# Performance work log

Measured on AMD Instinct MI355X. Metric: run time of the kernel, lower is better.

## Reference

```python
import jax, jax.numpy as jnp
import numpy as np

# Static architecture constants (from init_kwargs)
NUM_AREAS = 4
E_PER = 512          # excitatory units per area
I_PER = 128          # inhibitory units per area
H = NUM_AREAS * (E_PER + I_PER)   # 2560 hidden units
E_SIZE = NUM_AREAS * E_PER        # 2048 = int(0.8 * H)
NUM_OBJS = 2
IN_UNITS = 64
IN_SIZE = NUM_OBJS * IN_UNITS     # 128
ALPHA = 0.02 / 0.1                # dt_x / tau_x


def _build_masks():
    # Recurrent block-connectivity: tridiagonal area graph (adjacent areas connected)
    rec = np.eye(NUM_AREAS) + np.eye(NUM_AREAS, k=1) + np.eye(NUM_AREAS, k=-1)
    ee = np.kron(rec, np.ones((E_PER, E_PER)))
    ie = np.kron(rec, np.ones((I_PER, E_PER)))
    ei = np.kron(np.eye(NUM_AREAS), np.ones((E_PER, I_PER)))
    ii = np.kron(np.eye(NUM_AREAS), np.ones((I_PER, I_PER)))
    conn_rec = np.block([[ee, ei], [ie, ii]])  # rows/cols ordered [all-E | all-I]
    # Dale sign mask: first E_SIZE columns excitatory (+1), rest inhibitory (-1)
    sign = np.concatenate([np.ones(E_SIZE), -np.ones(H - E_SIZE)])[None, :]
    mask_rec = conn_rec * sign
    np.fill_diagonal(mask_rec, 0.0)  # remove_diag=True in h2h EILinear
    # Input connectivity: only area 0 receives external input (e_prop=1 -> all +1)
    in_mask = np.zeros((NUM_AREAS, NUM_OBJS)); in_mask[0, :] = 1.0
    in_e = np.kron(in_mask, np.ones((E_PER, IN_UNITS)))
    in_i = np.kron(in_mask, np.ones((I_PER, IN_UNITS)))
    mask_in = np.vstack([in_e, in_i])
    return jnp.asarray(mask_rec, jnp.float32), jnp.asarray(mask_in, jnp.float32)

MASK_REC, MASK_IN = _build_masks()


def retanh(x):
    return jnp.tanh(jax.nn.relu(x))


def setup_inputs() -> dict:
    key = jax.random.key(0)
    k1, k2, k3 = jax.random.split(key, 3)
    T, B = 32, 64
    x = jax.random.normal(k1, (T, B, IN_SIZE), dtype=jnp.float32)
    # positive-ish inits (original uses gamma; scale ~ 1/sqrt(fan-in))
    W_in = jax.random.uniform(k2, (H, IN_SIZE), dtype=jnp.float32) * 0.02
    W_rec = jax.random.uniform(k3, (H, H), dtype=jnp.float32) * (1.0 / np.sqrt(H))
    b_rec = jnp.zeros((H,), jnp.float32)
    state0 = jnp.zeros((B, H), jnp.float32)
    return {"x": x, "W_in": W_in, "W_rec": W_rec, "b_rec": b_rec, "state0": state0}


def reference(x, W_in, W_rec, b_rec, state0):
    # Effective weights: pos_function='abs' applied to raw weights, then sign/conn mask
    Wr = jnp.abs(W_rec) * MASK_REC          # [H, H]
    Wi = jnp.abs(W_in) * MASK_IN            # [H, IN_SIZE]

    def step(state, xt):
        out = retanh(state)                                # activation of old state
        total = out @ Wr.T + jax.nn.relu(xt) @ Wi.T + b_rec  # h2h(output) + x2h(relu(x)) + bias
        new_state = state * (1.0 - ALPHA) + ALPHA * total    # leaky integration (sigma=0)
        return new_state, retanh(new_state)

    _, outputs = jax.lax.scan(step, state0, x)  # outputs: [T, B, H]
    return outputs
```

## Files before the change

### kernel.cpp

```cpp
#include <hip/hip_runtime.h>
#include <math.h>

#define HH   2560
#define ESZ  2048
#define BB   64
#define TT   32
#define INSZ 128
constexpr float ALPHA_C = 0.2f;

typedef unsigned short ushort_t;
typedef __attribute__((ext_vector_type(8))) unsigned short u16x8;
typedef __attribute__((ext_vector_type(4))) float f32x4;

__device__ __forceinline__ float retanh_f(float v) { return tanhf(fmaxf(v, 0.f)); }
__device__ __forceinline__ ushort_t f2bf(float f) {
    unsigned u = __float_as_uint(f);
    return (ushort_t)((u + 0x7fffu + ((u >> 16) & 1u)) >> 16);
}

__device__ __forceinline__ int area_ne(int a)  { return (a == 1 || a == 2) ? 1536 : 1024; }
__device__ __forceinline__ int area_elo(int a) { return (a > 0 ? a - 1 : 0) << 9; }

__global__ __launch_bounds__(256) void wf_pack8(const float* __restrict__ Wrec,
                                                const float* __restrict__ Win,
                                                ushort_t* __restrict__ WF) {
    int idx = blockIdx.x * 256 + threadIdx.x;
    int l = idx & 63;
    int t = idx >> 6;
    int kc = t % 52, mt = t / 52;
    int area = mt / 40, local = mt - area * 40;
    int ridx = local * 16 + (l & 15);
    int h = (ridx < 512) ? ((area << 9) + ridx) : (ESZ + (area << 7) + (ridx - 512));
    int p0 = kc * 32 + ((l >> 4) << 3);
    int ne = area_ne(area), elo = area_elo(area);
    int nrec = ne + 128;
    int ntot = nrec + (area == 0 ? 128 : 0);
    u16x8 o;
#pragma unroll
    for (int j = 0; j < 8; j++) {
        int p = p0 + j;
        float w = 0.f;
        if (p < ne)        { int c = elo + p;                      w = (c == h) ? 0.f :  fabsf(Wrec[(size_t)h * HH + c]); }
        else if (p < nrec) { int c = ESZ + (area << 7) + (p - ne); w = (c == h) ? 0.f : -fabsf(Wrec[(size_t)h * HH + c]); }
        else if (p < ntot) { w = fabsf(Win[(size_t)h * INSZ + (p - nrec)]); }
        o[j] = f2bf(w);
    }
    *(u16x8*)(WF + ((size_t)t * 512 + l * 8)) = o;
}

__global__ __launch_bounds__(256) void xf_pack(const float* __restrict__ x,
                                               ushort_t* __restrict__ xF) {
    int idx = blockIdx.x * 256 + threadIdx.x;
    int j = idx & 7, l = (idx >> 3) & 63;
    int nt = (idx >> 9) & 3, kc = (idx >> 11) & 3, t = idx >> 13;
    int b = nt * 16 + (l & 15);
    int k = kc * 32 + ((l >> 4) << 3) + j;
    xF[idx] = f2bf(fmaxf(x[((size_t)t * BB + b) * INSZ + k], 0.f));
}

__device__ __forceinline__ void act_store(ushort_t* actF, int a, int p, int b, ushort_t v) {
    int kc = p >> 5, kk = p & 31;
    int lane = ((kk >> 3) << 4) + (b & 15);
    actF[(((a * 52 + kc) << 2) + (b >> 4)) * 512 + lane * 8 + (kk & 7)] = v;
}
__device__ __forceinline__ void scatter_act(ushort_t* actF, int h, int b, ushort_t v) {
    if (h < ESZ) {
        int ae = h >> 9;
        int alo = ae > 0 ? ae - 1 : 0, ahi = ae < 3 ? ae + 1 : 3;
        for (int a = alo; a <= ahi; a++) act_store(actF, a, h - area_elo(a), b, v);
    } else {
        int ai = (h - ESZ) >> 7;
        act_store(actF, ai, area_ne(ai) + (h - (ESZ + (ai << 7))), b, v);
    }
}

__global__ __launch_bounds__(256) void init3(const float* __restrict__ state0,
                                             float* __restrict__ stateT,
                                             ushort_t* __restrict__ actF) {
    int idx = blockIdx.x * 256 + threadIdx.x;
    int b = idx / HH, h = idx - b * HH;
    float s = state0[idx];
    int r = (h < ESZ) ? ((h >> 9) * 640 + (h & 511))
                      : (((h - ESZ) >> 7) * 640 + 512 + ((h - ESZ) & 127));
    stateT[r * BB + b] = s;
    scatter_act(actF, h, b, f2bf(retanh_f(s)));
}

__global__ __launch_bounds__(256) void step9(
    const ushort_t* __restrict__ WF,
    const ushort_t* __restrict__ actF_in,
    ushort_t* __restrict__ actF_out,
    const ushort_t* __restrict__ xFt,
    const float* __restrict__ brec,
    float* __restrict__ stateT,
    float* __restrict__ out_t)
{
    __shared__ float part[4 * 256];
    const int tid = threadIdx.x, lane = tid & 63, wv = tid >> 6;
    const int bid = blockIdx.x;
    const int area = (bid >> 1) & 3;
    const int nt   = ((bid >> 2) & 2) | (bid & 1);
    const int ml   = bid >> 4;
    const int mt   = area * 40 + ml;
    const int r0   = area * 640 + ml * 16;

    f32x4 acc = {0.f, 0.f, 0.f, 0.f};
    const ushort_t* aptr = WF + ((size_t)mt * 52 + wv) * 512 + lane * 8;
    const ushort_t* bptr = actF_in + (((size_t)area * 52 + wv) * 4 + nt) * 512 + lane * 8;
    const ushort_t* xptr = xFt + ((wv * 4) + nt) * 512 + lane * 8;

#define KLOOP(NIT, HASX)                                                     \
    {                                                                        \
        u16x8 af[NIT], bf[NIT];                                              \
        _Pragma("unroll")                                                    \
        for (int i = 0; i < (NIT); i++) {                                    \
            af[i] = *(const u16x8*)(aptr + (size_t)i * 2048);                \
            bf[i] = ((HASX) && i == (NIT) - 1)                               \
                        ? *(const u16x8*)xptr                                \
                        : *(const u16x8*)(bptr + (size_t)i * 8192);          \
        }                                                                    \
        _Pragma("unroll")                                                    \
        for (int i = 0; i < (NIT); i++)                                      \
            asm volatile("v_mfma_f32_16x16x32_bf16 %0, %1, %2, %0"           \
                         : "+v"(acc) : "v"(af[i]), "v"(bf[i]));              \
    }

    if (area == 0)      KLOOP(10, true)
    else if (area == 3) KLOOP(9,  false)
    else                KLOOP(13, false)
#undef KLOOP

    asm volatile("s_nop 7\n\ts_nop 7" : "+v"(acc));

#pragma unroll
    for (int i = 0; i < 4; i++)
        part[wv * 256 + (lane & 15) * 16 + ((lane >> 4) << 2) + i] = acc[i];
    __syncthreads();

    {
        const int mm = tid & 15, nn = tid >> 4;
        float s = part[nn * 16 + mm] + part[256 + nn * 16 + mm]
                + part[512 + nn * 16 + mm] + part[768 + nn * 16 + mm];
        const int b = nt * 16 + nn;
        const int ridx = ml * 16 + mm;
        const int h = (ridx < 512) ? ((area << 9) + ridx)
                                   : (ESZ + (area << 7) + (ridx - 512));
        const int r = r0 + mm;
        float st = stateT[r * BB + b];
        float ns = st * (1.f - ALPHA_C) + ALPHA_C * (s + brec[h]);
        stateT[r * BB + b] = ns;
        float o = retanh_f(ns);
        out_t[(size_t)b * HH + h] = o;
        scatter_act(actF_out, h, b, f2bf(o));
    }
}

__device__ __forceinline__ void area_params(int area, int& e_lo, int& n_e,
                                            int& i_lo, int& n_rec, int& n_tot) {
    e_lo = (area > 0 ? area - 1 : 0) << 9;
    int e_hi = ((area < 3 ? area + 1 : 3) + 1) << 9;
    n_e = e_hi - e_lo;
    i_lo = ESZ + (area << 7);
    n_rec = n_e + 128;
    n_tot = n_rec + (area == 0 ? INSZ : 0);
}
__device__ __forceinline__ int row_h(int area, int idx) {
    return (idx < 512) ? ((area << 9) + idx) : (ESZ + (area << 7) + (idx - 512));
}
__global__ __launch_bounds__(256) void init_state2(const float* __restrict__ state0,
                                                   float* __restrict__ stateT,
                                                   float* __restrict__ act0) {
    int idx = blockIdx.x * 256 + threadIdx.x;
    int b = idx / HH, h = idx - b * HH;
    float s = state0[idx];
    int r = (h < ESZ) ? ((h >> 9) * 640 + (h & 511))
                      : (((h - ESZ) >> 7) * 640 + 512 + ((h - ESZ) & 127));
    stateT[r * BB + b] = s;
    act0[((h >> 1) << 7) + b * 2 + (h & 1)] = retanh_f(s);
}
__global__ __launch_bounds__(1024, 4) void step_raw(
    const float* __restrict__ W, const float* __restrict__ Win,
    const float* __restrict__ brec, const float* __restrict__ x_t,
    const float* __restrict__ actIn, float* __restrict__ actOut,
    float* __restrict__ stateT, float* __restrict__ out_t)
{
    __shared__ float part[16 * 680];
    const int tid = threadIdx.x, lane = tid & 63, wv = tid >> 6;
    const int area = blockIdx.x >> 6;
    const int rb = (blockIdx.x & 63) * 10;
    int e_lo, n_e, i_lo, n_rec, n_tot;
    area_params(area, e_lo, n_e, i_lo, n_rec, n_tot);
    const int r0 = area * 640 + rb;
    const int C = n_tot >> 4;
    float2 acc[10];
#pragma unroll
    for (int j = 0; j < 10; j++) acc[j] = make_float2(0.f, 0.f);
    for (int c = wv; c < C; c += 16) {
        const int p0 = c << 4;
        float2 av[8];
        int cbase;
        if (p0 < n_rec) {
            cbase = (p0 < n_e) ? (e_lo + p0) : (i_lo + (p0 - n_e));
            const float* ap = actIn + ((cbase >> 1) << 7) + lane * 2;
#pragma unroll
            for (int i = 0; i < 8; i++) av[i] = *(const float2*)(ap + (i << 7));
        } else {
            cbase = -1;
            const int k0 = p0 - n_rec;
            const float4* xp = (const float4*)(x_t + lane * INSZ + k0);
#pragma unroll
            for (int q = 0; q < 4; q++) {
                float4 v = xp[q];
                av[2 * q]     = make_float2(fmaxf(v.x, 0.f), fmaxf(v.y, 0.f));
                av[2 * q + 1] = make_float2(fmaxf(v.z, 0.f), fmaxf(v.w, 0.f));
            }
        }
#pragma unroll
        for (int j = 0; j < 10; j++) {
            const int h = row_h(area, rb + j);
            const float sgn = (cbase >= 0 && p0 >= n_e) ? -1.f : 1.f;
            const float* wr = (cbase >= 0) ? (W + (size_t)h * HH + cbase)
                                           : (Win + (size_t)h * INSZ + (p0 - n_rec));
#pragma unroll
            for (int i = 0; i < 8; i++) {
                acc[j].x = fmaf(sgn * fabsf(wr[2 * i]),     av[i].x, acc[j].x);
                acc[j].y = fmaf(sgn * fabsf(wr[2 * i + 1]), av[i].y, acc[j].y);
            }
        }
    }
#pragma unroll
    for (int j = 0; j < 10; j++)
        part[wv * 680 + j * 68 + lane] = acc[j].x + acc[j].y;
    __syncthreads();
    int j = -1, b = 0;
    if (tid < 512)      { b = tid >> 3;      j = tid & 7; }
    else if (tid < 640) { int u = tid - 512; b = u >> 1;  j = 8 + (u & 1); }
    if (j >= 0) {
        const int h = row_h(area, rb + j);
        float s = 0.f;
#pragma unroll
        for (int w16 = 0; w16 < 16; w16++) s += part[w16 * 680 + j * 68 + b];
        float sgn = (h < ESZ) ? 1.f : -1.f;
        s -= sgn * fabsf(W[(size_t)h * HH + h]) * actIn[((h >> 1) << 7) + b * 2 + (h & 1)];
        const int r = r0 + j;
        float st = stateT[r * BB + b];
        float ns = st * (1.f - ALPHA_C) + ALPHA_C * (s + brec[h]);
        stateT[r * BB + b] = ns;
        float o = retanh_f(ns);
        out_t[(size_t)b * HH + h] = o;
        actOut[((h >> 1) << 7) + b * 2 + (h & 1)] = o;
    }
}

extern "C" void kernel_launch(void* const* d_in, const int* in_sizes, int n_in,
                              void* d_out, int out_size, void* d_ws, size_t ws_size,
                              hipStream_t stream) {
    const float* x      = (const float*)d_in[0];
    const float* W_in   = (const float*)d_in[1];
    const float* W_rec  = (const float*)d_in[2];
    const float* b_rec  = (const float*)d_in[3];
    const float* state0 = (const float*)d_in[4];
    float* out = (float*)d_out;

    const size_t WFn = (size_t)160 * 52 * 512;
    const size_t xFn = (size_t)TT * 8192;
    const size_t aFn = (size_t)4 * 52 * 4 * 512;
    const size_t need = (WFn + xFn + 2 * aFn) * 2 + (size_t)HH * BB * 4;

    if (ws_size >= need) {
        ushort_t* WF   = (ushort_t*)d_ws;
        ushort_t* xF   = WF + WFn;
        ushort_t* actA = xF + xFn;
        ushort_t* actB = actA + aFn;
        float* stateT  = (float*)(actB + aFn);

        wf_pack8<<<2080, 256, 0, stream>>>(W_rec, W_in, WF);
        xf_pack<<<1024, 256, 0, stream>>>(x, xF);
        init3<<<640, 256, 0, stream>>>(state0, stateT, actA);
        for (int t = 0; t < TT; t++) {
            ushort_t* ai = (t & 1) ? actB : actA;
            ushort_t* ao = (t & 1) ? actA : actB;
            step9<<<640, 256, 0, stream>>>(WF, ai, ao, xF + (size_t)t * 8192,
                                           b_rec, stateT, out + (size_t)t * BB * HH);
        }
    } else {
        float* ws = (float*)d_ws;
        const size_t bufElems = (size_t)HH * BB;
        float* stateT = ws;
        float* actA   = stateT + bufElems;
        float* actB   = actA + bufElems;
        init_state2<<<(BB * HH) / 256, 256, 0, stream>>>(state0, stateT, actA);
        for (int t = 0; t < TT; t++) {
            const float* ai = (t & 1) ? actB : actA;
            float* ao       = (t & 1) ? actA : actB;
            step_raw<<<256, 1024, 0, stream>>>(W_rec, W_in, b_rec,
                                               x + (size_t)t * BB * INSZ,
                                               ai, ao, stateT, out + (size_t)t * BB * HH);
        }
    }
}
```

Measured before the change: 286.9 us.

## Fuse all timesteps into one persistent kernel with flag-based grid barrier

Replaces the 32 per-timestep launches with a single persistent kernel of 160 blocks, one per 16-row M tile. Each block covers all four batch tiles and keeps its weight fragments and state in registers across steps. Steps are synchronised through per-block release flags polled with agent-scope atomics. This removes launch overhead and repeated weight and state loads, at the cost of fewer blocks (less parallelism), a spin-wait barrier with a guard limit, and reliance on all 160 blocks being co-resident.

```diff
diff --git a/kernel.cpp b/kernel.cpp
--- a/kernel.cpp
+++ b/kernel.cpp
@@ -76,7 +76,10 @@
 
 __global__ __launch_bounds__(256) void init3(const float* __restrict__ state0,
                                              float* __restrict__ stateT,
-                                             ushort_t* __restrict__ actF) {
+                                             ushort_t* __restrict__ actF,
+                                             unsigned* __restrict__ flags) {
+    if (blockIdx.x == 0 && threadIdx.x < 192)
+        flags[threadIdx.x] = (threadIdx.x < 160) ? 0u : 0xFFFFFFFFu;
     int idx = blockIdx.x * 256 + threadIdx.x;
     int b = idx / HH, h = idx - b * HH;
     float s = state0[idx];
@@ -86,73 +89,127 @@
     scatter_act(actF, h, b, f2bf(retanh_f(s)));
 }
 
-__global__ __launch_bounds__(256) void step9(
+template<int NIT, bool HASX>
+__device__ __forceinline__ void run_steps(
     const ushort_t* __restrict__ WF,
-    const ushort_t* __restrict__ actF_in,
-    ushort_t* __restrict__ actF_out,
-    const ushort_t* __restrict__ xFt,
-    const float* __restrict__ brec,
-    float* __restrict__ stateT,
-    float* __restrict__ out_t)
+    ushort_t* __restrict__ actA, ushort_t* __restrict__ actB,
+    const ushort_t* __restrict__ xF, const float* __restrict__ brec,
+    const float* __restrict__ stateT, float* __restrict__ out,
+    unsigned* __restrict__ flags, float* part, int mt, int area)
 {
-    __shared__ float part[4 * 256];
     const int tid = threadIdx.x, lane = tid & 63, wv = tid >> 6;
-    const int bid = blockIdx.x;
-    const int area = (bid >> 1) & 3;
-    const int nt   = ((bid >> 2) & 2) | (bid & 1);
-    const int ml   = bid >> 4;
-    const int mt   = area * 40 + ml;
-    const int r0   = area * 640 + ml * 16;
-
-    f32x4 acc = {0.f, 0.f, 0.f, 0.f};
-    const ushort_t* aptr = WF + ((size_t)mt * 52 + wv) * 512 + lane * 8;
-    const ushort_t* bptr = actF_in + (((size_t)area * 52 + wv) * 4 + nt) * 512 + lane * 8;
-    const ushort_t* xptr = xFt + ((wv * 4) + nt) * 512 + lane * 8;
-
-#define KLOOP(NIT, HASX)                                                     \
-    {                                                                        \
-        u16x8 af[NIT], bf[NIT];                                              \
-        _Pragma("unroll")                                                    \
-        for (int i = 0; i < (NIT); i++) {                                    \
-            af[i] = *(const u16x8*)(aptr + (size_t)i * 2048);                \
-            bf[i] = ((HASX) && i == (NIT) - 1)                               \
-                        ? *(const u16x8*)xptr                                \
-                        : *(const u16x8*)(bptr + (size_t)i * 8192);          \
-        }                                                                    \
-        _Pragma("unroll")                                                    \
-        for (int i = 0; i < (NIT); i++)                                      \
-            asm volatile("v_mfma_f32_16x16x32_bf16 %0, %1, %2, %0"           \
-                         : "+v"(acc) : "v"(af[i]), "v"(bf[i]));              \
-    }
-
-    if (area == 0)      KLOOP(10, true)
-    else if (area == 3) KLOOP(9,  false)
-    else                KLOOP(13, false)
-#undef KLOOP
-
-    asm volatile("s_nop 7\n\ts_nop 7" : "+v"(acc));
-
-#pragma unroll
-    for (int i = 0; i < 4; i++)
-        part[wv * 256 + (lane & 15) * 16 + ((lane >> 4) << 2) + i] = acc[i];
-    __syncthreads();
-
+    const int ml = mt - area * 40;
+
+    u16x8 af[NIT];
     {
-        const int mm = tid & 15, nn = tid >> 4;
-        float s = part[nn * 16 + mm] + part[256 + nn * 16 + mm]
-                + part[512 + nn * 16 + mm] + part[768 + nn * 16 + mm];
-        const int b = nt * 16 + nn;
-        const int ridx = ml * 16 + mm;
-        const int h = (ridx < 512) ? ((area << 9) + ridx)
-                                   : (ESZ + (area << 7) + (ridx - 512));
-        const int r = r0 + mm;
-        float st = stateT[r * BB + b];
-        float ns = st * (1.f - ALPHA_C) + ALPHA_C * (s + brec[h]);
-        stateT[r * BB + b] = ns;
-        float o = retanh_f(ns);
-        out_t[(size_t)b * HH + h] = o;
-        scatter_act(actF_out, h, b, f2bf(o));
-    }
+        const ushort_t* aptr = WF + ((size_t)mt * 52 + wv) * 512 + lane * 8;
+#pragma unroll
+        for (int i = 0; i < NIT; i++) af[i] = *(const u16x8*)(aptr + (size_t)i * 2048);
+    }
+
+    const int mm = tid & 15, nn = tid >> 4;
+    const int ridx = ml * 16 + mm;
+    const int h = (ridx < 512) ? ((area << 9) + ridx) : (ESZ + (area << 7) + (ridx - 512));
+    const int r = area * 640 + ml * 16 + mm;
+    const float bh = brec[h];
+    float st[4];
+#pragma unroll
+    for (int nt = 0; nt < 4; nt++) st[nt] = stateT[r * BB + nt * 16 + nn];
+
+    const size_t boff = (((size_t)area * 52 + wv) * 4) * 512 + lane * 8;
+    ushort_t* bApt = actA + boff;
+    ushort_t* bBpt = actB + boff;
+    const ushort_t* xw = xF + (size_t)(wv * 4) * 512 + lane * 8;
+
+    for (int t = 0; t < TT; t++) {
+        const ushort_t* bin = (t & 1) ? bBpt : bApt;
+        ushort_t* aout      = (t & 1) ? actA : actB;
+        const ushort_t* xt  = xw + (size_t)t * 8192;
+
+        f32x4 acc[4];
+#pragma unroll
+        for (int g = 0; g < 4; g++) acc[g] = (f32x4){0.f, 0.f, 0.f, 0.f};
+
+#pragma unroll
+        for (int g = 0; g < 4; g++) {
+            u16x8 bf[NIT];
+#pragma unroll
+            for (int i = 0; i < NIT; i++)
+                bf[i] = (HASX && i == NIT - 1)
+                            ? *(const u16x8*)(xt + g * 512)
+                            : *(const u16x8*)(bin + g * 512 + (size_t)i * 8192);
+#pragma unroll
+            for (int i = 0; i < NIT; i++)
+                asm volatile("v_mfma_f32_16x16x32_bf16 %0, %1, %2, %0"
+                             : "+v"(acc[g]) : "v"(af[i]), "v"(bf[i]));
+        }
+        asm volatile("s_nop 7\n\ts_nop 7");
+
+#pragma unroll
+        for (int g = 0; g < 4; g++)
+            *(f32x4*)(part + (size_t)(wv * 4 + g) * 256 + (lane & 15) * 16 + ((lane >> 4) << 2)) = acc[g];
+        __syncthreads();
+
+        float* out_t = out + (size_t)t * BB * HH;
+#pragma unroll
+        for (int nt = 0; nt < 4; nt++) {
+            float s = 0.f;
+#pragma unroll
+            for (int w = 0; w < 4; w++) s += part[(w * 4 + nt) * 256 + nn * 16 + mm];
+            float ns = st[nt] * (1.f - ALPHA_C) + ALPHA_C * (s + bh);
+            st[nt] = ns;
+            float o = retanh_f(ns);
+            const int b = nt * 16 + nn;
+            out_t[(size_t)b * HH + h] = o;
+            scatter_act(aout, h, b, f2bf(o));
+        }
+
+        if (t < TT - 1) {
+            __syncthreads();
+            if (tid == 0)
+                __hip_atomic_store(flags + mt, (unsigned)(t + 1),
+                                   __ATOMIC_RELEASE, __HIP_MEMORY_SCOPE_AGENT);
+            if (wv == 0) {
+                const unsigned long long* f64 = (const unsigned long long*)flags;
+                const unsigned tgt = (unsigned)(t + 1);
+                bool done = false;
+                int guard = 0;
+                while (!done && guard < (1 << 20)) {
+                    unsigned long long v0 = __hip_atomic_load(f64 + lane,
+                                        __ATOMIC_RELAXED, __HIP_MEMORY_SCOPE_AGENT);
+                    unsigned long long v1 = 0xFFFFFFFFFFFFFFFFull;
+                    if (lane < 32)
+                        v1 = __hip_atomic_load(f64 + 64 + lane,
+                                        __ATOMIC_RELAXED, __HIP_MEMORY_SCOPE_AGENT);
+                    bool ok = ((unsigned)v0 >= tgt) && ((unsigned)(v0 >> 32) >= tgt)
+                           && ((unsigned)v1 >= tgt) && ((unsigned)(v1 >> 32) >= tgt);
+                    done = (__all(ok) != 0);
+                    guard++;
+                }
+            }
+            __syncthreads();
+            __builtin_amdgcn_fence(__ATOMIC_ACQUIRE, "agent");
+            __builtin_amdgcn_sched_barrier(0);
+        }
+    }
+}
+
+__global__ __launch_bounds__(256) void step_all(
+    const ushort_t* __restrict__ WF,
+    ushort_t* __restrict__ actA, ushort_t* __restrict__ actB,
+    const ushort_t* __restrict__ xF, const float* __restrict__ brec,
+    const float* __restrict__ stateT, float* __restrict__ out,
+    unsigned* __restrict__ flags)
+{
+    __shared__ float part[4 * 4 * 256];
+    const int mt = blockIdx.x;
+    const int area = mt / 40;
+    if (area == 0)
+        run_steps<10, true >(WF, actA, actB, xF, brec, stateT, out, flags, part, mt, 0);
+    else if (area == 3)
+        run_steps<9,  false>(WF, actA, actB, xF, brec, stateT, out, flags, part, mt, 3);
+    else
+        run_steps<13, false>(WF, actA, actB, xF, brec, stateT, out, flags, part, mt, area);
 }
 
 __device__ __forceinline__ void area_params(int area, int& e_lo, int& n_e,
@@ -265,7 +322,7 @@
     const size_t WFn = (size_t)160 * 52 * 512;
     const size_t xFn = (size_t)TT * 8192;
     const size_t aFn = (size_t)4 * 52 * 4 * 512;
-    const size_t need = (WFn + xFn + 2 * aFn) * 2 + (size_t)HH * BB * 4;
+    const size_t need = (WFn + xFn + 2 * aFn) * 2 + (size_t)HH * BB * 4 + 192 * 4;
 
     if (ws_size >= need) {
         ushort_t* WF   = (ushort_t*)d_ws;
@@ -273,16 +330,12 @@
         ushort_t* actA = xF + xFn;
         ushort_t* actB = actA + aFn;
         float* stateT  = (float*)(actB + aFn);
+        unsigned* flags = (unsigned*)(stateT + (size_t)HH * BB);
 
         wf_pack8<<<2080, 256, 0, stream>>>(W_rec, W_in, WF);
         xf_pack<<<1024, 256, 0, stream>>>(x, xF);
-        init3<<<640, 256, 0, stream>>>(state0, stateT, actA);
-        for (int t = 0; t < TT; t++) {
-            ushort_t* ai = (t & 1) ? actB : actA;
-            ushort_t* ao = (t & 1) ? actA : actB;
-            step9<<<640, 256, 0, stream>>>(WF, ai, ao, xF + (size_t)t * 8192,
-                                           b_rec, stateT, out + (size_t)t * BB * HH);
-        }
+        init3<<<640, 256, 0, stream>>>(state0, stateT, actA, flags);
+        step_all<<<160, 256, 0, stream>>>(WF, actA, actB, xF, b_rec, stateT, out, flags);
     } else {
         float* ws = (float*)d_ws;
         const size_t bufElems = (size_t)HH * BB;
```

Measured after the change: 587.6 us. +104.8%, slower.
